# Kernel tuning notes

Measured on AMD Instinct MI355X. Metric: run time of the kernel, lower is better.

Reference implementation:

```python
import jax, jax.numpy as jnp
import numpy as np

NUM_FEATS = 65536
IN_SIZE = 1024
OUT_SIZE = 1024
NUM_MODULES = 8


def setup_inputs() -> dict:
    key = jax.random.key(0)
    k1, k2, k3, k4 = jax.random.split(key, 4)
    in_feats = jax.random.normal(k1, (NUM_FEATS, IN_SIZE), dtype=jnp.float32)
    module_ids = jax.random.randint(k2, (NUM_FEATS,), 0, NUM_MODULES, dtype=jnp.int64)
    # Per-expert Linear parameters (same architecture, different weights).
    # PyTorch nn.Linear default init: U(-1/sqrt(in), 1/sqrt(in)).
    bound = 1.0 / np.sqrt(IN_SIZE)
    W = jax.random.uniform(k3, (NUM_MODULES, IN_SIZE, OUT_SIZE), jnp.float32, -bound, bound)
    b = jax.random.uniform(k4, (NUM_MODULES, OUT_SIZE), jnp.float32, -bound, bound)
    return {"in_feats": in_feats, "module_ids": module_ids, "W": W, "b": b}


def reference(in_feats, module_ids, W, b):
    # Faithful to: out[mask_e] = Linear_e(in_feats[mask_e]) for each expert e.
    # Vectorized as a fixed small loop over experts with masked combine
    # (no Python loop over the data dimension).
    num_feats = in_feats.shape[0]
    out = jnp.zeros((num_feats, OUT_SIZE), dtype=in_feats.dtype)
    for e in range(NUM_MODULES):
        y = in_feats @ W[e] + b[e]  # [num_feats, OUT_SIZE]
        mask = (module_ids == e)[:, None]
        out = jnp.where(mask, y, out)
    return out
```

## Files before the change

kernel.cpp:

```cpp
#include <hip/hip_runtime.h>

typedef unsigned short u16;
typedef unsigned int u32;
typedef __attribute__((ext_vector_type(8))) short short8;
typedef __attribute__((ext_vector_type(4))) float f32x4;

#define NF 65536
#define KDIM 1024
#define NDIM 1024
#define NE 8
#define BM 128
#define BN 128
#define MAX_MT (NF / BM + NE)
#define GEMM_GRID (MAX_MT * 8)
#define TILE_B 16384
#define SORT_BLOCKS 64

#define AS1 __attribute__((address_space(1)))
#define AS3 __attribute__((address_space(3)))

__device__ __forceinline__ u16 f2bf(float f) {
  u32 u = __float_as_uint(f);
  u += 0x7FFF + ((u >> 16) & 1);
  return (u16)(u >> 16);
}

__device__ __forceinline__ int swz8(int r) {
  return (r & 7) ^ ((r >> 3) & 7);
}
__device__ __forceinline__ int swz_slot(int r) { return swz8(r) << 4; }
__device__ __forceinline__ int amsk(int r) {
  return (swz8(r) << 1) | (r & 1);
}

__device__ __forceinline__ void cp16(void* l, const void* g) {
  __builtin_amdgcn_global_load_lds((const AS1 unsigned int*)g,
                                   (AS3 unsigned int*)l, 16, 0, 0);
}

__device__ __forceinline__ u32 cvtpk(float a, float b) {
  u32 r;
  asm("v_cvt_pk_bf16_f32 %0, %1, %2" : "=v"(r) : "v"(a), "v"(b));
  return r;
}

__global__ void k_cnt(const int* __restrict__ ids, int* __restrict__ gcnt) {
  __shared__ int wc[16][NE];
  int b = blockIdx.x, t = threadIdx.x;
  int w = t >> 6, lane = t & 63;
  if (t < 16 * NE) ((int*)wc)[t] = 0;
  __syncthreads();
  for (int s = 0; s < 4; ++s) {
    int i = (b << 10) + (s << 8) + t;
    int e = ids[i];
#pragma unroll
    for (int ee = 0; ee < NE; ++ee) {
      unsigned long long mask = __ballot(e == ee);
      if (lane == 0) wc[(s << 2) + w][ee] = (int)__popcll(mask);
    }
  }
  __syncthreads();
  if (t < NE) {
    int sum = 0;
#pragma unroll
    for (int j = 0; j < 16; ++j) sum += wc[j][t];
    gcnt[b * NE + t] = sum;
  }
}

__global__ void k_excl(const int* __restrict__ gcnt, int* __restrict__ counts,
                       int* __restrict__ offsets, int* __restrict__ tile_base,
                       int* __restrict__ base) {
  __shared__ int tot[NE], offs[NE];
  int t = threadIdx.x;
  if (t < NE) {
    int s = 0;
    for (int b = 0; b < SORT_BLOCKS; ++b) s += gcnt[b * NE + t];
    tot[t] = s;
    counts[t] = s;
  }
  __syncthreads();
  if (t == 0) {
    int run = 0, tb = 0;
    tile_base[0] = 0;
    for (int e = 0; e < NE; ++e) {
      offsets[e] = run;
      offs[e] = run;
      run += tot[e];
      tb += (tot[e] + BM - 1) / BM;
      tile_base[e + 1] = tb;
    }
  }
  __syncthreads();
  if (t < NE) {
    int run = offs[t];
    for (int b = 0; b < SORT_BLOCKS; ++b) {
      base[b * NE + t] = run;
      run += gcnt[b * NE + t];
    }
  }
}

__global__ void k_place(const int* __restrict__ ids, const int* __restrict__ base,
                        int* __restrict__ perm) {
  __shared__ int wc[16][NE], wsc[16][NE];
  int b = blockIdx.x, t = threadIdx.x;
  int w = t >> 6, lane = t & 63;
  for (int s = 0; s < 4; ++s) {
    int i = (b << 10) + (s << 8) + t;
    int e = ids[i];
#pragma unroll
    for (int ee = 0; ee < NE; ++ee) {
      unsigned long long mask = __ballot(e == ee);
      if (lane == 0) wc[(s << 2) + w][ee] = (int)__popcll(mask);
    }
  }
  __syncthreads();
  if (t < NE) {
    int run = 0;
#pragma unroll
    for (int j = 0; j < 16; ++j) {
      wsc[j][t] = run;
      run += wc[j][t];
    }
  }
  __syncthreads();
  for (int s = 0; s < 4; ++s) {
    int i = (b << 10) + (s << 8) + t;
    int e = ids[i];
#pragma unroll
    for (int ee = 0; ee < NE; ++ee) {
      unsigned long long mask = __ballot(e == ee);
      if (e == ee) {
        int rank = (int)__popcll(mask & ((1ull << lane) - 1ull));
        perm[base[b * NE + e] + wsc[(s << 2) + w][e] + rank] = i;
      }
    }
  }
}

__global__ void k_wconv2(const float* __restrict__ W, u16* __restrict__ Wt) {
  int b = blockIdx.x;
  int e = b >> 7, nt = (b >> 4) & 7, kt = b & 15;
  int tid = threadIdx.x;
  const float* We = W + ((size_t)e << 20);
  char* dst = (char*)Wt + (size_t)b * TILE_B;
#pragma unroll
  for (int i = 0; i < 4; ++i) {
    int o = (i << 12) + (tid << 4);
    int r = o >> 7;
    int s = ((o >> 4) & 7) ^ swz8(r);
    int n = (nt << 7) + r;
    int k = (kt << 6) + (s << 3);
    u32 p[4];
#pragma unroll
    for (int j = 0; j < 4; ++j) {
      u32 lo = f2bf(We[(size_t)(k + 2 * j) * NDIM + n]);
      u32 hi = f2bf(We[(size_t)(k + 2 * j + 1) * NDIM + n]);
      p[j] = lo | (hi << 16);
    }
    *(uint4*)(dst + o) = make_uint4(p[0], p[1], p[2], p[3]);
  }
}

__global__ __launch_bounds__(256, 3) void k_gemm_fused(
    const float* __restrict__ A, const u16* __restrict__ Wt,
    const float* __restrict__ bias, const int* __restrict__ perm,
    const int* __restrict__ offsets, const int* __restrict__ counts,
    const int* __restrict__ tile_base, float* __restrict__ out) {
  int bid = blockIdx.x;
  const int cpx = GEMM_GRID >> 3;
  int l = (bid & 7) * cpx + (bid >> 3);
  int mt = l >> 3, nt = l & 7;
  if (mt >= tile_base[NE]) return;
  int e = 0;
#pragma unroll
  for (int ee = 0; ee < NE - 1; ++ee)
    if (mt >= tile_base[ee + 1]) e = ee + 1;
  int mloc = mt - tile_base[e];
  int row_base = offsets[e] + (mloc << 7);
  int rim = counts[e] - (mloc << 7);
  rim = rim < BM ? rim : BM;
  int n0 = nt << 7;

  __shared__ __align__(16) char ldsA[BM * 64 * 4];
  __shared__ __align__(16) char ldsB[BN * 64 * 2];

  int tid = threadIdx.x;
  int lane = tid & 63, wid = tid >> 6;
  int wr = wid >> 1, wc = wid & 1;
  int l15 = lane & 15;
  int q4 = lane >> 4;
  int lk2 = q4 << 4;

  u32 aoff[8];
#pragma unroll
  for (int j = 0; j < 8; ++j) {
    int r = (wid << 5) + (j << 2) + q4;
    int rr = r < rim ? r : rim - 1;
    int g = perm[row_base + rr];
    int t = l15 ^ amsk(r);
    aoff[j] = ((u32)g << 12) + ((u32)t << 4);
  }
  int adst = (wid << 13) + (lane << 4);
  const char* Ab = (const char*)A;

  const char* srcB = (const char*)Wt + (size_t)(((e << 3) + nt) << 4) * TILE_B;
  int toff = tid << 4;

  int ar_addr[4];
#pragma unroll
  for (int m = 0; m < 4; ++m) {
    int r = (wr << 6) + (m << 4) + l15;
    ar_addr[m] = (r << 8) + (((q4 << 1) ^ amsk(r)) << 4);
  }
  int br_addr[4];
#pragma unroll
  for (int n = 0; n < 4; ++n) {
    int r = (wc << 6) + (n << 4) + l15;
    br_addr[n] = (r << 7) + (lk2 ^ swz_slot(r));
  }

  f32x4 acc[4][4];
#pragma unroll
  for (int m = 0; m < 4; ++m)
#pragma unroll
    for (int n = 0; n < 4; ++n) acc[m][n] = f32x4{0.f, 0.f, 0.f, 0.f};

#pragma unroll 1
  for (int kt = 0; kt < KDIM / 64; ++kt) {
    __syncthreads();
    u32 kb = (u32)kt << 8;
#pragma unroll
    for (int j = 0; j < 8; ++j)
      cp16(ldsA + adst + (j << 10), Ab + (aoff[j] + kb));
    const char* gb = srcB + ((size_t)kt << 14);
#pragma unroll
    for (int j = 0; j < 4; ++j) cp16(ldsB + toff + (j << 12), gb + toff + (j << 12));
    asm volatile("s_waitcnt vmcnt(0)" ::: "memory");
    __builtin_amdgcn_sched_barrier(0);
    __syncthreads();
#pragma unroll
    for (int kk = 0; kk < 2; ++kk) {
      short8 af[4], bfr[4];
#pragma unroll
      for (int m = 0; m < 4; ++m) {
        int a0 = ar_addr[m] ^ (kk << 7);
        f32x4 lo = *(const f32x4*)(ldsA + a0);
        f32x4 hi = *(const f32x4*)(ldsA + (a0 ^ 16));
        u32 p0 = cvtpk(lo[0], lo[1]);
        u32 p1 = cvtpk(lo[2], lo[3]);
        u32 p2 = cvtpk(hi[0], hi[1]);
        u32 p3 = cvtpk(hi[2], hi[3]);
        af[m] = __builtin_bit_cast(short8, make_uint4(p0, p1, p2, p3));
      }
#pragma unroll
      for (int n = 0; n < 4; ++n)
        bfr[n] = __builtin_bit_cast(short8,
                                    *(const uint4*)(ldsB + (br_addr[n] ^ (kk << 6))));
#pragma unroll
      for (int m = 0; m < 4; ++m)
#pragma unroll
        for (int n = 0; n < 4; ++n)
          acc[m][n] = __builtin_amdgcn_mfma_f32_16x16x32_bf16(af[m], bfr[n],
                                                              acc[m][n], 0, 0, 0);
    }
  }

  float bv[4];
#pragma unroll
  for (int n = 0; n < 4; ++n)
    bv[n] = bias[(e << 10) + n0 + (wc << 6) + (n << 4) + l15];
  int rq = (lane >> 4) << 2;
#pragma unroll
  for (int m = 0; m < 4; ++m) {
#pragma unroll
    for (int j = 0; j < 4; ++j) {
      int rl = (wr << 6) + (m << 4) + rq + j;
      if (rl < rim) {
        int grow = perm[row_base + rl];
        float* orow = out + (size_t)grow * NDIM + n0 + (wc << 6) + l15;
#pragma unroll
        for (int n = 0; n < 4; ++n) orow[n << 4] = acc[m][n][j] + bv[n];
      }
    }
  }
}

__global__ __launch_bounds__(256, 3) void k_gemm_slow(
    const float* __restrict__ A, const float* __restrict__ W,
    const float* __restrict__ bias, const int* __restrict__ perm,
    const int* __restrict__ offsets, const int* __restrict__ counts,
    const int* __restrict__ tile_base, float* __restrict__ out) {
  int bid = blockIdx.x;
  const int cpx = GEMM_GRID >> 3;
  int l = (bid & 7) * cpx + (bid >> 3);
  int mt = l >> 3, nt = l & 7;
  if (mt >= tile_base[NE]) return;
  int e = 0;
#pragma unroll
  for (int ee = 0; ee < NE - 1; ++ee)
    if (mt >= tile_base[ee + 1]) e = ee + 1;
  int mloc = mt - tile_base[e];
  int row_base = offsets[e] + (mloc << 7);
  int rim = counts[e] - (mloc << 7);
  rim = rim < BM ? rim : BM;
  int n0 = nt << 7;

  __shared__ u16 Al[BM * 64];
  __shared__ u16 Bl[BN * 64];
  char* alb = (char*)Al;
  char* blb = (char*)Bl;

  int tid = threadIdx.x;
  int lane = tid & 63, wid = tid >> 6;
  int wr = wid >> 1, wc = wid & 1;
  int l15 = lane & 15;
  int lk2 = (lane >> 4) << 4;

  int acol4 = tid & 15, argp = tid >> 4;
  const float* arow_p[8];
  int aswz[8];
#pragma unroll
  for (int i = 0; i < 8; ++i) {
    int r = argp + (i << 4);
    int rr = r < rim ? r : rim - 1;
    int grow = perm[row_base + rr];
    arow_p[i] = A + (size_t)grow * KDIM + (acol4 << 2);
    aswz[i] = r * 128 + ((acol4 << 3) ^ swz_slot(r));
  }
  int bnloc = tid & 127;
  int bkh = tid >> 7;
  const float* bcol_f = W + ((size_t)e << 20) + n0 + bnloc;
  int bswz[4];
#pragma unroll
  for (int j = 0; j < 4; ++j)
    bswz[j] = bnloc * 128 + (((bkh << 6) + (j << 4)) ^ swz_slot(bnloc));

  int ar_addr[4], br_addr[4];
#pragma unroll
  for (int m = 0; m < 4; ++m) {
    int r = (wr << 6) + (m << 4) + l15;
    ar_addr[m] = r * 128 + (lk2 ^ swz_slot(r));
  }
#pragma unroll
  for (int n = 0; n < 4; ++n) {
    int r = (wc << 6) + (n << 4) + l15;
    br_addr[n] = r * 128 + (lk2 ^ swz_slot(r));
  }

  f32x4 acc[4][4];
#pragma unroll
  for (int m = 0; m < 4; ++m)
#pragma unroll
    for (int n = 0; n < 4; ++n) acc[m][n] = f32x4{0.f, 0.f, 0.f, 0.f};

#pragma unroll 1
  for (int kt = 0; kt < KDIM / 64; ++kt) {
    int k0 = kt << 6;
    __syncthreads();
#pragma unroll
    for (int i = 0; i < 8; ++i) {
      float4 v = *(const float4*)(arow_p[i] + k0);
      u32 lo = (u32)f2bf(v.x) | ((u32)f2bf(v.y) << 16);
      u32 hi = (u32)f2bf(v.z) | ((u32)f2bf(v.w) << 16);
      *(uint2*)(alb + aswz[i]) = make_uint2(lo, hi);
    }
    float vv[32];
#pragma unroll
    for (int i = 0; i < 32; ++i)
      vv[i] = bcol_f[(size_t)(k0 + (bkh << 5) + i) << 10];
#pragma unroll
    for (int j = 0; j < 4; ++j) {
      uint4 pkt;
      pkt.x = (u32)f2bf(vv[j * 8 + 0]) | ((u32)f2bf(vv[j * 8 + 1]) << 16);
      pkt.y = (u32)f2bf(vv[j * 8 + 2]) | ((u32)f2bf(vv[j * 8 + 3]) << 16);
      pkt.z = (u32)f2bf(vv[j * 8 + 4]) | ((u32)f2bf(vv[j * 8 + 5]) << 16);
      pkt.w = (u32)f2bf(vv[j * 8 + 6]) | ((u32)f2bf(vv[j * 8 + 7]) << 16);
      *(uint4*)(blb + bswz[j]) = pkt;
    }
    __syncthreads();
#pragma unroll
    for (int kk = 0; kk < 2; ++kk) {
      int kx = kk << 6;
      short8 af[4], bfr[4];
#pragma unroll
      for (int m = 0; m < 4; ++m)
        af[m] = __builtin_bit_cast(short8, *(const uint4*)(alb + (ar_addr[m] ^ kx)));
#pragma unroll
      for (int n = 0; n < 4; ++n)
        bfr[n] = __builtin_bit_cast(short8, *(const uint4*)(blb + (br_addr[n] ^ kx)));
#pragma unroll
      for (int m = 0; m < 4; ++m)
#pragma unroll
        for (int n = 0; n < 4; ++n)
          acc[m][n] = __builtin_amdgcn_mfma_f32_16x16x32_bf16(af[m], bfr[n],
                                                              acc[m][n], 0, 0, 0);
    }
  }

  float bv[4];
#pragma unroll
  for (int n = 0; n < 4; ++n)
    bv[n] = bias[(e << 10) + n0 + (wc << 6) + (n << 4) + l15];
  int rq = (lane >> 4) << 2;
#pragma unroll
  for (int m = 0; m < 4; ++m) {
#pragma unroll
    for (int j = 0; j < 4; ++j) {
      int rl = (wr << 6) + (m << 4) + rq + j;
      if (rl < rim) {
        int grow = perm[row_base + rl];
        float* orow = out + (size_t)grow * NDIM + n0 + (wc << 6) + l15;
#pragma unroll
        for (int n = 0; n < 4; ++n) orow[n << 4] = acc[m][n][j] + bv[n];
      }
    }
  }
}

extern "C" void kernel_launch(void* const* d_in, const int* in_sizes, int n_in,
                              void* d_out, int out_size, void* d_ws,
                              size_t ws_size, hipStream_t stream) {
  const float* A = (const float*)d_in[0];
  const int* ids = (const int*)d_in[1];
  const float* W = (const float*)d_in[2];
  const float* bias = (const float*)d_in[3];
  float* out = (float*)d_out;

  char* ws = (char*)d_ws;
  int* counts = (int*)ws;
  int* offsets = (int*)(ws + 32);
  int* tile_base = (int*)(ws + 64);
  int* gcnt = (int*)(ws + 128);
  int* base = (int*)(ws + 2176);
  int* perm = (int*)(ws + 8192);
  const size_t wt_off = 524288;
  const size_t wt_sz = (size_t)NE * 8 * 16 * TILE_B;
  u16* Wt = (u16*)(ws + wt_off);
  bool fast = ws_size >= wt_off + wt_sz;

  k_cnt<<<SORT_BLOCKS, 256, 0, stream>>>(ids, gcnt);
  k_excl<<<1, 64, 0, stream>>>(gcnt, counts, offsets, tile_base, base);
  k_place<<<SORT_BLOCKS, 256, 0, stream>>>(ids, base, perm);
  if (fast) {
    k_wconv2<<<NE * 8 * 16, 256, 0, stream>>>(W, Wt);
    k_gemm_fused<<<GEMM_GRID, 256, 0, stream>>>(A, Wt, bias, perm, offsets,
                                                counts, tile_base, out);
  } else {
    k_gemm_slow<<<GEMM_GRID, 256, 0, stream>>>(A, W, bias, perm, offsets,
                                               counts, tile_base, out);
  }
}
```

Baseline: 297.1 us.

## Load A fragments directly to registers and double-buffer B tiles in LDS

The A (fp32 activation) tile no longer goes through LDS. Each lane loads its MFMA fragment straight from global memory into registers via the permuted row pointers. The B weight tile is double-buffered in LDS so the next k-tile's async load is issued before the current compute, and one __syncthreads per iteration is removed. This cuts LDS traffic and footprint, which may allow higher occupancy, but A global loads become uncoalesced (each lane reads 32 bytes of a separate row) and are still waited on with vmcnt(0) each iteration.

```diff
diff --git a/kernel.cpp b/kernel.cpp
--- a/kernel.cpp
+++ b/kernel.cpp
@@ -29,9 +29,6 @@
   return (r & 7) ^ ((r >> 3) & 7);
 }
 __device__ __forceinline__ int swz_slot(int r) { return swz8(r) << 4; }
-__device__ __forceinline__ int amsk(int r) {
-  return (swz8(r) << 1) | (r & 1);
-}
 
 __device__ __forceinline__ void cp16(void* l, const void* g) {
   __builtin_amdgcn_global_load_lds((const AS1 unsigned int*)g,
@@ -183,8 +180,7 @@
   rim = rim < BM ? rim : BM;
   int n0 = nt << 7;
 
-  __shared__ __align__(16) char ldsA[BM * 64 * 4];
-  __shared__ __align__(16) char ldsB[BN * 64 * 2];
+  __shared__ __align__(16) char ldsB[2][TILE_B];
 
   int tid = threadIdx.x;
   int lane = tid & 63, wid = tid >> 6;
@@ -193,27 +189,18 @@
   int q4 = lane >> 4;
   int lk2 = q4 << 4;
 
-  u32 aoff[8];
-#pragma unroll
-  for (int j = 0; j < 8; ++j) {
-    int r = (wid << 5) + (j << 2) + q4;
+  const float* ap[4];
+#pragma unroll
+  for (int m = 0; m < 4; ++m) {
+    int r = (wr << 6) + (m << 4) + l15;
     int rr = r < rim ? r : rim - 1;
     int g = perm[row_base + rr];
-    int t = l15 ^ amsk(r);
-    aoff[j] = ((u32)g << 12) + ((u32)t << 4);
-  }
-  int adst = (wid << 13) + (lane << 4);
-  const char* Ab = (const char*)A;
+    ap[m] = A + (size_t)g * KDIM + (q4 << 3);
+  }
 
   const char* srcB = (const char*)Wt + (size_t)(((e << 3) + nt) << 4) * TILE_B;
   int toff = tid << 4;
 
-  int ar_addr[4];
-#pragma unroll
-  for (int m = 0; m < 4; ++m) {
-    int r = (wr << 6) + (m << 4) + l15;
-    ar_addr[m] = (r << 8) + (((q4 << 1) ^ amsk(r)) << 4);
-  }
   int br_addr[4];
 #pragma unroll
   for (int n = 0; n < 4; ++n) {
@@ -227,37 +214,46 @@
 #pragma unroll
     for (int n = 0; n < 4; ++n) acc[m][n] = f32x4{0.f, 0.f, 0.f, 0.f};
 
+#pragma unroll
+  for (int j = 0; j < 4; ++j) cp16(&ldsB[0][0] + toff + (j << 12), srcB + toff + (j << 12));
+
 #pragma unroll 1
   for (int kt = 0; kt < KDIM / 64; ++kt) {
-    __syncthreads();
-    u32 kb = (u32)kt << 8;
-#pragma unroll
-    for (int j = 0; j < 8; ++j)
-      cp16(ldsA + adst + (j << 10), Ab + (aoff[j] + kb));
-    const char* gb = srcB + ((size_t)kt << 14);
-#pragma unroll
-    for (int j = 0; j < 4; ++j) cp16(ldsB + toff + (j << 12), gb + toff + (j << 12));
+    if (kt < KDIM / 64 - 1) {
+      const char* gb = srcB + ((size_t)(kt + 1) << 14);
+      char* lb = &ldsB[(kt + 1) & 1][0];
+#pragma unroll
+      for (int j = 0; j < 4; ++j) cp16(lb + toff + (j << 12), gb + toff + (j << 12));
+    }
+    f32x4 av[4][2][2];
+    int koff = kt << 6;
+#pragma unroll
+    for (int m = 0; m < 4; ++m)
+#pragma unroll
+      for (int kk = 0; kk < 2; ++kk) {
+        const float* p = ap[m] + koff + (kk << 5);
+        av[m][kk][0] = *(const f32x4*)p;
+        av[m][kk][1] = *(const f32x4*)(p + 4);
+      }
     asm volatile("s_waitcnt vmcnt(0)" ::: "memory");
     __builtin_amdgcn_sched_barrier(0);
     __syncthreads();
+    const char* lb = &ldsB[kt & 1][0];
 #pragma unroll
     for (int kk = 0; kk < 2; ++kk) {
       short8 af[4], bfr[4];
 #pragma unroll
       for (int m = 0; m < 4; ++m) {
-        int a0 = ar_addr[m] ^ (kk << 7);
-        f32x4 lo = *(const f32x4*)(ldsA + a0);
-        f32x4 hi = *(const f32x4*)(ldsA + (a0 ^ 16));
-        u32 p0 = cvtpk(lo[0], lo[1]);
-        u32 p1 = cvtpk(lo[2], lo[3]);
-        u32 p2 = cvtpk(hi[0], hi[1]);
-        u32 p3 = cvtpk(hi[2], hi[3]);
+        u32 p0 = cvtpk(av[m][kk][0][0], av[m][kk][0][1]);
+        u32 p1 = cvtpk(av[m][kk][0][2], av[m][kk][0][3]);
+        u32 p2 = cvtpk(av[m][kk][1][0], av[m][kk][1][1]);
+        u32 p3 = cvtpk(av[m][kk][1][2], av[m][kk][1][3]);
         af[m] = __builtin_bit_cast(short8, make_uint4(p0, p1, p2, p3));
       }
 #pragma unroll
       for (int n = 0; n < 4; ++n)
         bfr[n] = __builtin_bit_cast(short8,
-                                    *(const uint4*)(ldsB + (br_addr[n] ^ (kk << 6))));
+                                    *(const uint4*)(lb + (br_addr[n] ^ (kk << 6))));
 #pragma unroll
       for (int m = 0; m < 4; ++m)
 #pragma unroll
```

Result: slower. 592.6 us (+99.4%).
